# Performance work log

Hardware: AMD Instinct MI355X
Metric: run time of the kernel (lower is better)

## Reference

```python
import jax, jax.numpy as jnp
import numpy as np

B, S, H = 32768, 16, 16  # batch, seq_len, G_hiddensize (code requires H == S and H == latent_dim == 16)
LATENT = 16
DISC_DIMS = [(1, 32), (32, 16), (16, 8), (8, 16), (16, 32)]


def setup_inputs() -> dict:
    key = jax.random.key(0)
    ks = iter(jax.random.split(key, 64))
    def p(shape, scale=0.1):
        return (jax.random.normal(next(ks), shape, dtype=jnp.float32) * scale)
    inp = dict(
        values=jax.random.normal(next(ks), (B, S), dtype=jnp.float32),
        masks=jax.random.randint(next(ks), (B, S), 0, 2).astype(jnp.int32),
        g_fwd_Wih=p((4 * H, 1)), g_fwd_Whh=p((4 * H, H)), g_fwd_b=p((4 * H,)),
        g_bwd_Wih=p((4 * H, 1)), g_bwd_Whh=p((4 * H, H)), g_bwd_b=p((4 * H,)),
        imp_W=p((1, H)), imp_b=p((1,)),
        fc_W=p((LATENT, H)), fc_b=p((LATENT,)),
        dec_Wih=p((4 * H, LATENT)), dec_Whh=p((4 * H, H)), dec_b=p((4 * H,)),
        dec_out_W=p((1, H)), dec_out_b=p((1,)),
        disc_out_W=p((1, 32)), disc_out_b=p((1,)),
    )
    for k, (i, h) in enumerate(DISC_DIMS):
        inp[f"d_W_{k}"] = p((4 * h, i))
        inp[f"d_b_{k}"] = p((4 * h,))
    return inp


def lstm_cell(x, h, c, Wih, Whh, b):
    gates = x @ Wih.T + h @ Whh.T + b
    i, f, g, o = jnp.split(gates, 4, axis=-1)
    c = jax.nn.sigmoid(f) * c + jax.nn.sigmoid(i) * jnp.tanh(g)
    h = jax.nn.sigmoid(o) * jnp.tanh(c)
    return h, c


def _forward(values, masks, g_fwd_Wih, g_fwd_Whh, g_fwd_b, g_bwd_Wih, g_bwd_Whh, g_bwd_b,
             imp_W, imp_b, fc_W, fc_b, dec_Wih, dec_Whh, dec_b, dec_out_W, dec_out_b,
             disc_out_W, disc_out_b,
             d_W_0, d_b_0, d_W_1, d_b_1, d_W_2, d_b_2, d_W_3, d_b_3, d_W_4, d_b_4):
    dt = values.dtype
    Bsz = values.shape[0]
    x = values[:, :, None]                     # (B, S, 1)
    m = masks.astype(dt)[:, :, None]           # (B, S, 1)
    # NOTE: torch.flip along axis 2 (size 1) is a no-op, so the bwd cell sees the
    # same (un-reversed) sequence as the fwd cell -- faithfully reproduced here.
    zH = jnp.zeros((Bsz, H), dt)
    h_f, c_f = lstm_cell(jnp.full((Bsz, 1), 128.0, dt), zH, zH, g_fwd_Wih, g_fwd_Whh, g_fwd_b)
    h_b, c_b = lstm_cell(jnp.full((Bsz, 1), -128.0, dt), zH, zH, g_bwd_Wih, g_bwd_Whh, g_bwd_b)

    def gen_step(carry, xm):
        h_f, c_f, h_b, c_b = carry
        x_t, m_t = xm                          # (B,1) each
        cc_f = (1 - m_t) * x_t + m_t * (h_f @ imp_W.T + imp_b)
        cc_b = (1 - m_t) * x_t + m_t * (h_b @ imp_W.T + imp_b)
        h_f, c_f = lstm_cell(cc_f, h_f, c_f, g_fwd_Wih, g_fwd_Whh, g_fwd_b)
        h_b, c_b = lstm_cell(cc_b, h_b, c_b, g_bwd_Wih, g_bwd_Whh, g_bwd_b)
        return (h_f, c_f, h_b, c_b), None

    (h_f, c_f, h_b, c_b), _ = jax.lax.scan(
        gen_step, (h_f, c_f, h_b, c_b),
        (jnp.transpose(x, (1, 0, 2)), jnp.transpose(m, (1, 0, 2))))
    h = h_f + h_b                               # (B, H), H == S
    imputations = h.reshape(Bsz, S, 1)
    imputed = imputations * (1 - m) + x * m      # (B, S, 1)

    # Discriminator: torch calls each LSTMCell WITHOUT state every timestep, so
    # hidden/cell start at zero each call -> purely feedforward per (batch, t).
    # W_hh @ 0 == 0, so only W_ih and the combined bias matter. Vectorize over B*S.
    inp = imputed.reshape(Bsz * S, 1)
    for W, b in ((d_W_0, d_b_0), (d_W_1, d_b_1), (d_W_2, d_b_2), (d_W_3, d_b_3), (d_W_4, d_b_4)):
        gates = inp @ W.T + b
        i, f, g, o = jnp.split(gates, 4, axis=-1)
        cc = jax.nn.sigmoid(i) * jnp.tanh(g)
        inp = jax.nn.sigmoid(o) * jnp.tanh(cc)
    disc_output = (inp @ disc_out_W.T + disc_out_b).reshape(Bsz, S, 1)

    latent = h @ fc_W.T + fc_b                  # (B, 16)

    # Decoder: ignores latent values (only uses batch size); start token = 128s.
    hd = cd = jnp.zeros((Bsz, H), dt)
    hd, cd = lstm_cell(jnp.full((Bsz, LATENT), 128.0, dt), hd, cd, dec_Wih, dec_Whh, dec_b)

    def dec_step(carry, _):
        hd, cd = carry
        hd, cd = lstm_cell(cd, hd, cd, dec_Wih, dec_Whh, dec_b)
        return (hd, cd), hd @ dec_out_W.T + dec_out_b

    _, outs = jax.lax.scan(dec_step, (hd, cd), None, length=S)  # (S, B, 1)
    reconstructed = jnp.transpose(outs, (1, 0, 2))
    return imputed, disc_output, latent, reconstructed


def reference(values, masks, g_fwd_Wih, g_fwd_Whh, g_fwd_b, g_bwd_Wih, g_bwd_Whh, g_bwd_b,
              imp_W, imp_b, fc_W, fc_b, dec_Wih, dec_Whh, dec_b, dec_out_W, dec_out_b,
              disc_out_W, disc_out_b,
              d_W_0, d_b_0, d_W_1, d_b_1, d_W_2, d_b_2, d_W_3, d_b_3, d_W_4, d_b_4):
    return _forward(values, masks, g_fwd_Wih, g_fwd_Whh, g_fwd_b, g_bwd_Wih, g_bwd_Whh, g_bwd_b,
                    imp_W, imp_b, fc_W, fc_b, dec_Wih, dec_Whh, dec_b, dec_out_W, dec_out_b,
                    disc_out_W, disc_out_b,
                    d_W_0, d_b_0, d_W_1, d_b_1, d_W_2, d_b_2, d_W_3, d_b_3, d_W_4, d_b_4)
```

## Files before the change

kernel.cpp:

```cpp
#include <hip/hip_runtime.h>

#define BB 32768
#define BS (BB*16)

typedef __attribute__((ext_vector_type(8))) short bf8v;
typedef __attribute__((ext_vector_type(4))) float f4v;

#define RECO 64
#define TAB  128
#define NTAB 2049
#define HFO  8448
#define HBO  (HFO+BS)

#define PW0 0
#define PB0 96
#define PW1 192
#define PB1 1920
#define PW2 1968
#define PB2 2448
#define PW3 2472
#define PB3 3048
#define PW4 3096
#define PB4 5016
#define POW 5112
#define POB 5144
#define PN  5148

#define NSCAN 1024
#define NTABB 129
#define DECB  (NSCAN + NTABB)

__device__ __forceinline__ float sigm(float x){
    return __builtin_amdgcn_rcpf(1.f + __expf(-x));
}
__device__ __forceinline__ float tanh_f(float x){
    return 1.f - 2.f * __builtin_amdgcn_rcpf(1.f + __expf(2.f * x));
}
__device__ __forceinline__ float dunit(float gi, float gg, float go){
    return sigm(go) * tanh_f(sigm(gi) * tanh_f(gg));
}
__device__ __forceinline__ unsigned short f2bf(float f){
    union { float f; unsigned int i; } v; v.f = f;
    unsigned int x = v.i;
    unsigned int r = x + 0x7fffu + ((x >> 16) & 1u);
    return (unsigned short)(r >> 16);
}

struct P29 { const float* p[29]; };

__device__ __forceinline__ bf8v makeB(const float* Whh, const float* Wih,
                                      int row, int quad)
{
    bf8v B = {0,0,0,0,0,0,0,0};
    if (quad < 2) {
        const float4* p = (const float4*)(Whh + row*16 + quad*8);
        float4 a0 = p[0], a1 = p[1];
        B[0]=(short)f2bf(a0.x); B[1]=(short)f2bf(a0.y);
        B[2]=(short)f2bf(a0.z); B[3]=(short)f2bf(a0.w);
        B[4]=(short)f2bf(a1.x); B[5]=(short)f2bf(a1.y);
        B[6]=(short)f2bf(a1.z); B[7]=(short)f2bf(a1.w);
    } else if (quad == 2) {
        B[0] = (short)f2bf(Wih[row]);
    }
    return B;
}

__global__ __launch_bounds__(256)
void k_main(P29 a, const int* __restrict__ masks, float* __restrict__ ws)
{
    __shared__ __align__(16) float smem[PN];
    int tid = threadIdx.x;

    if (blockIdx.x < NSCAN) {
        int lane = tid & 63;
        int wv   = tid >> 6;
        int n    = lane & 15;
        int quad = lane >> 4;
        int dir  = (int)(blockIdx.x >= 512);
        int gid0 = blockIdx.x * 64 + wv * 16;
        int b0   = gid0 & 32767;
        float* wbase = smem + wv * 656;
        float* xs    = wbase;
        int*   msI   = (int*)(wbase + 256);
        unsigned short* hbp = (unsigned short*)(wbase + 512);
        float* ccf   = wbase + 640;
        const int4* hbI = (const int4*)hbp;
        {
            size_t gbase = (size_t)b0 * 16;
            int e = lane * 4;
            float4 xv = *(const float4*)(a.p[0] + gbase + e);
            int4   mv = *(const int4*)(masks + gbase + e);
            int sm = lane >> 2;
            int st = (lane & 3) * 4;
            xs[(st+0)*16 + sm] = xv.x;  msI[(st+0)*16 + sm] = mv.x;
            xs[(st+1)*16 + sm] = xv.y;  msI[(st+1)*16 + sm] = mv.y;
            xs[(st+2)*16 + sm] = xv.z;  msI[(st+2)*16 + sm] = mv.z;
            xs[(st+3)*16 + sm] = xv.w;  msI[(st+3)*16 + sm] = mv.w;
        }
        const float* __restrict__ Wih = a.p[2 + 3*dir];
        const float* __restrict__ Whh = a.p[3 + 3*dir];
        const float* __restrict__ bia = a.p[4 + 3*dir];
        bf8v Bi = makeB(Whh, Wih, n,      quad);
        bf8v Bf = makeB(Whh, Wih, 16+n,   quad);
        bf8v Bg = makeB(Whh, Wih, 32+n,   quad);
        bf8v Bo = makeB(Whh, Wih, 48+n,   quad);
        bf8v Bp = {0,0,0,0,0,0,0,0};
        if (quad < 2) {
            const float4* p = (const float4*)(a.p[8] + quad*8);
            float4 a0 = p[0], a1 = p[1];
            Bp[0]=(short)f2bf(a0.x); Bp[1]=(short)f2bf(a0.y);
            Bp[2]=(short)f2bf(a0.z); Bp[3]=(short)f2bf(a0.w);
            Bp[4]=(short)f2bf(a1.x); Bp[5]=(short)f2bf(a1.y);
            Bp[6]=(short)f2bf(a1.z); Bp[7]=(short)f2bf(a1.w);
        }
        float impb = a.p[9][0];
        float bi_ = bia[n], bf_ = bia[16+n], bg_ = bia[32+n], bo_ = bia[48+n];
        float sgn = dir ? -128.f : 128.f;
        float c0, h0;
        {
            float gi0 = sgn*Wih[n]    + bi_;
            float gg0 = sgn*Wih[32+n] + bg_;
            float go0 = sgn*Wih[48+n] + bo_;
            c0 = sigm(gi0) * tanh_f(gg0);
            h0 = sigm(go0) * tanh_f(c0);
        }
        float c[4] = {c0, c0, c0, c0};
        float h[4];
        {
            unsigned short hb0 = f2bf(h0);
            #pragma unroll
            for (int r = 0; r < 4; r++) hbp[(quad*4+r)*16 + n] = hb0;
        }
        const f4v cz = {0.f, 0.f, 0.f, 0.f};
        const bf8v Az = {0,0,0,0,0,0,0,0};
        for (int t = 0; t < 16; t++) {
            union { int4 i4; bf8v b; } au;
            au.i4 = hbI[(n << 1) | (quad & 1)];
            bf8v A = (quad < 2) ? au.b : Az;
            f4v dimp = __builtin_amdgcn_mfma_f32_16x16x32_bf16(A, Bp, cz, 0, 0, 0);
            float4 xt4 = *(const float4*)(xs + t*16 + quad*4);
            int4   mt4 = *(const int4*)(msI + t*16 + quad*4);
            float cc0 = mt4.x ? (dimp[0] + impb) : xt4.x;
            float cc1 = mt4.y ? (dimp[1] + impb) : xt4.y;
            float cc2 = mt4.z ? (dimp[2] + impb) : xt4.z;
            float cc3 = mt4.w ? (dimp[3] + impb) : xt4.w;
            if (n == 0) {
                ccf[quad*4+0] = cc0; ccf[quad*4+1] = cc1;
                ccf[quad*4+2] = cc2; ccf[quad*4+3] = cc3;
            }
            if (quad == 2) A[0] = (short)f2bf(ccf[n]);
            f4v di = __builtin_amdgcn_mfma_f32_16x16x32_bf16(A, Bi, cz, 0, 0, 0);
            f4v df = __builtin_amdgcn_mfma_f32_16x16x32_bf16(A, Bf, cz, 0, 0, 0);
            f4v dg = __builtin_amdgcn_mfma_f32_16x16x32_bf16(A, Bg, cz, 0, 0, 0);
            f4v dO = __builtin_amdgcn_mfma_f32_16x16x32_bf16(A, Bo, cz, 0, 0, 0);
            #pragma unroll
            for (int r = 0; r < 4; r++) {
                float gi = di[r] + bi_;
                float gf = df[r] + bf_;
                float gg = dg[r] + bg_;
                float go = dO[r] + bo_;
                float cn = sigm(gf)*c[r] + sigm(gi)*tanh_f(gg);
                c[r] = cn;
                float hh = sigm(go)*tanh_f(cn);
                h[r] = hh;
                hbp[(quad*4+r)*16 + n] = f2bf(hh);
            }
        }
        float* outp = ws + HFO + (size_t)dir*BS + (size_t)b0*16;
        #pragma unroll
        for (int r = 0; r < 4; r++) outp[(quad*4+r)*16 + n] = h[r];
        return;
    }

    if (blockIdx.x < DECB) {
        float* wl = smem;
#define STAGE(WS, BSi, h, K, padK, wdst, bdst) \
    { const float* Wp = a.p[WS]; const float* Bp2 = a.p[BSi]; \
      for (int i = tid; i < 3*(h)*(K); i += 256){ \
        int r = i/(K), k = i - r*(K); int g = r/(h), u0 = r - g*(h); \
        int sr = (g==0? u0 : (g==1? 2*(h)+u0 : 3*(h)+u0)); \
        wl[(wdst) + r*(padK) + k] = Wp[sr*(K) + k]; } \
      for (int i = tid; i < 3*(h); i += 256){ \
        int g = i/(h), u0 = i - g*(h); \
        int sr = (g==0? u0 : (g==1? 2*(h)+u0 : 3*(h)+u0)); \
        wl[(bdst) + i] = Bp2[sr]; } }
        STAGE(19, 20, 32,  1,  1, PW0, PB0)
        STAGE(21, 22, 16, 32, 36, PW1, PB1)
        STAGE(23, 24,  8, 16, 20, PW2, PB2)
        STAGE(25, 26, 16,  8, 12, PW3, PB3)
        STAGE(27, 28, 32, 16, 20, PW4, PB4)
#undef STAGE
        { const float* s = a.p[17]; for (int i = tid; i < 32; i += 256) wl[POW+i] = s[i]; }
        if (tid == 0) wl[POB] = a.p[18][0];
        __syncthreads();
        int u = tid & 15;
        int gbase = (tid & 63) & 48;
        int gid = (blockIdx.x - NSCAN) * 16 + (tid >> 4);
        const float4* w4 = (const float4*)wl;
        float xin = -8.f + (float)gid * (1.f/128.f);
        float lo = dunit(xin*wl[PW0+u]    + wl[PB0+u],
                         xin*wl[PW0+32+u] + wl[PB0+32+u],
                         xin*wl[PW0+64+u] + wl[PB0+64+u]);
        float hi = dunit(xin*wl[PW0+16+u] + wl[PB0+16+u],
                         xin*wl[PW0+48+u] + wl[PB0+48+u],
                         xin*wl[PW0+80+u] + wl[PB0+80+u]);
        float A0[32];
        #pragma unroll
        for (int k = 0; k < 16; k++) { A0[k] = __shfl(lo, gbase+k); A0[16+k] = __shfl(hi, gbase+k); }
        float gi = wl[PB1+u], gg = wl[PB1+16+u], go = wl[PB1+32+u];
        int bi_ = (PW1 + u*36)>>2, bg_ = (PW1 + (16+u)*36)>>2, bo_ = (PW1 + (32+u)*36)>>2;
        #pragma unroll
        for (int q = 0; q < 8; q++) {
            float4 wi = w4[bi_+q], wg = w4[bg_+q], wo = w4[bo_+q];
            float b0=A0[4*q], b1=A0[4*q+1], b2=A0[4*q+2], b3=A0[4*q+3];
            gi += b0*wi.x + b1*wi.y + b2*wi.z + b3*wi.w;
            gg += b0*wg.x + b1*wg.y + b2*wg.z + b3*wg.w;
            go += b0*wo.x + b1*wo.y + b2*wo.z + b3*wo.w;
        }
        float a1 = dunit(gi, gg, go);
        float A1[16];
        #pragma unroll
        for (int k = 0; k < 16; k++) A1[k] = __shfl(a1, gbase+k);
        int v = u & 7;
        gi = wl[PB2+v]; gg = wl[PB2+8+v]; go = wl[PB2+16+v];
        bi_ = (PW2 + v*20)>>2; bg_ = (PW2 + (8+v)*20)>>2; bo_ = (PW2 + (16+v)*20)>>2;
        #pragma unroll
        for (int q = 0; q < 4; q++) {
            float4 wi = w4[bi_+q], wg = w4[bg_+q], wo = w4[bo_+q];
            float b0=A1[4*q], b1=A1[4*q+1], b2=A1[4*q+2], b3=A1[4*q+3];
            gi += b0*wi.x + b1*wi.y + b2*wi.z + b3*wi.w;
            gg += b0*wg.x + b1*wg.y + b2*wg.z + b3*wg.w;
            go += b0*wo.x + b1*wo.y + b2*wo.z + b3*wo.w;
        }
        float a2 = dunit(gi, gg, go);
        float A2[8];
        #pragma unroll
        for (int k = 0; k < 8; k++) A2[k] = __shfl(a2, gbase+k);
        gi = wl[PB3+u]; gg = wl[PB3+16+u]; go = wl[PB3+32+u];
        bi_ = (PW3 + u*12)>>2; bg_ = (PW3 + (16+u)*12)>>2; bo_ = (PW3 + (32+u)*12)>>2;
        #pragma unroll
        for (int q = 0; q < 2; q++) {
            float4 wi = w4[bi_+q], wg = w4[bg_+q], wo = w4[bo_+q];
            float b0=A2[4*q], b1=A2[4*q+1], b2=A2[4*q+2], b3=A2[4*q+3];
            gi += b0*wi.x + b1*wi.y + b2*wi.z + b3*wi.w;
            gg += b0*wg.x + b1*wg.y + b2*wg.z + b3*wg.w;
            go += b0*wo.x + b1*wo.y + b2*wo.z + b3*wo.w;
        }
        float a3 = dunit(gi, gg, go);
        float A3[16];
        #pragma unroll
        for (int k = 0; k < 16; k++) A3[k] = __shfl(a3, gbase+k);
        float part;
        {
            float g0i = wl[PB4+u], g0g = wl[PB4+32+u], g0o = wl[PB4+64+u];
            float g1i = wl[PB4+16+u], g1g = wl[PB4+48+u], g1o = wl[PB4+80+u];
            int c0i = (PW4 + u*20)>>2,      c0g = (PW4 + (32+u)*20)>>2, c0o = (PW4 + (64+u)*20)>>2;
            int c1i = (PW4 + (16+u)*20)>>2, c1g = (PW4 + (48+u)*20)>>2, c1o = (PW4 + (80+u)*20)>>2;
            #pragma unroll
            for (int q = 0; q < 4; q++) {
                float b0=A3[4*q], b1=A3[4*q+1], b2=A3[4*q+2], b3=A3[4*q+3];
                float4 wi = w4[c0i+q], wg = w4[c0g+q], wo = w4[c0o+q];
                g0i += b0*wi.x + b1*wi.y + b2*wi.z + b3*wi.w;
                g0g += b0*wg.x + b1*wg.y + b2*wg.z + b3*wg.w;
                g0o += b0*wo.x + b1*wo.y + b2*wo.z + b3*wo.w;
                wi = w4[c1i+q]; wg = w4[c1g+q]; wo = w4[c1o+q];
                g1i += b0*wi.x + b1*wi.y + b2*wi.z + b3*wi.w;
                g1g += b0*wg.x + b1*wg.y + b2*wg.z + b3*wg.w;
                g1o += b0*wo.x + b1*wo.y + b2*wo.z + b3*wo.w;
            }
            part = dunit(g0i, g0g, g0o)*wl[POW+u] + dunit(g1i, g1g, g1o)*wl[POW+16+u];
        }
        part += __shfl_xor(part, 1);
        part += __shfl_xor(part, 2);
        part += __shfl_xor(part, 4);
        part += __shfl_xor(part, 8);
        if (u == 0 && gid < NTAB) ws[TAB + gid] = part + wl[POB];
        return;
    }

    {
        float* dh = smem;
        float* dc = smem + 16;
        const float* Wih = a.p[12];
        const float* Whh = a.p[13];
        const float* bb  = a.p[14];
        const float* oW  = a.p[15];
        const float* ob  = a.p[16];
        float wii[16], wff[16], wgg[16], woo[16];
        float vii[16], vff[16], vgg[16], voo[16];
        float bi_r=0, bf_r=0, bg_r=0, bo_r=0;
        if (tid < 16) {
            int uu = tid;
            #pragma unroll
            for (int k = 0; k < 16; k++) {
                wii[k]=Wih[uu*16+k];      vii[k]=Whh[uu*16+k];
                wff[k]=Wih[(16+uu)*16+k]; vff[k]=Whh[(16+uu)*16+k];
                wgg[k]=Wih[(32+uu)*16+k]; vgg[k]=Whh[(32+uu)*16+k];
                woo[k]=Wih[(48+uu)*16+k]; voo[k]=Whh[(48+uu)*16+k];
            }
            bi_r=bb[uu]; bf_r=bb[16+uu]; bg_r=bb[32+uu]; bo_r=bb[48+uu];
            float gi = bi_r, gg = bg_r, go = bo_r;
            #pragma unroll
            for (int k = 0; k < 16; k++) {
                gi += 128.f * wii[k];
                gg += 128.f * wgg[k];
                go += 128.f * woo[k];
            }
            float cd0 = sigm(gi) * tanh_f(gg);
            dc[tid] = cd0; dh[tid] = sigm(go) * tanh_f(cd0);
        }
        __syncthreads();
        for (int t = 0; t < 16; t++) {
            float rx[16], rh[16], cold = 0.f;
            if (tid < 16) {
                #pragma unroll
                for (int k = 0; k < 16; k++) { rx[k] = dc[k]; rh[k] = dh[k]; }
                cold = dc[tid];
            }
            __syncthreads();
            if (tid < 16) {
                float gi = bi_r, gf = bf_r, gg = bg_r, go = bo_r;
                #pragma unroll
                for (int k = 0; k < 16; k++) {
                    gi += rx[k]*wii[k] + rh[k]*vii[k];
                    gf += rx[k]*wff[k] + rh[k]*vff[k];
                    gg += rx[k]*wgg[k] + rh[k]*vgg[k];
                    go += rx[k]*woo[k] + rh[k]*voo[k];
                }
                float cn = sigm(gf)*cold + sigm(gi)*tanh_f(gg);
                dc[tid] = cn; dh[tid] = sigm(go)*tanh_f(cn);
            }
            __syncthreads();
            if (tid == 0) {
                float o = ob[0];
                #pragma unroll
                for (int k = 0; k < 16; k++) o += dh[k] * oW[k];
                ws[RECO + t] = o;
            }
            __syncthreads();
        }
    }
}

__global__ __launch_bounds__(256) void k_post(P29 a, const int* __restrict__ masks,
                                              const float* __restrict__ ws,
                                              float* __restrict__ out)
{
    __shared__ float tab[NTAB];
    __shared__ __align__(16) float fw[256];
    __shared__ __align__(16) float rec[16];
    __shared__ float fb[16];
    int tid = threadIdx.x;
    for (int i = tid; i < NTAB; i += 256) tab[i] = ws[TAB + i];
    fw[tid] = a.p[10][tid];
    if (tid < 16) { fb[tid] = a.p[11][tid]; rec[tid] = ws[RECO + tid]; }
    __syncthreads();
    int T = blockIdx.x * 256 + tid;
    int b = T >> 2;
    int q = T & 3;
    int tq = q * 4;
    const float4* hf4 = (const float4*)(ws + HFO + (size_t)b*16);
    const float4* hb4 = (const float4*)(ws + HBO + (size_t)b*16);
    float4 s0, s1, s2, s3;
    {
        float4 f0=hf4[0], f1=hf4[1], f2=hf4[2], f3=hf4[3];
        float4 g0=hb4[0], g1=hb4[1], g2=hb4[2], g3=hb4[3];
        s0 = make_float4(f0.x+g0.x, f0.y+g0.y, f0.z+g0.z, f0.w+g0.w);
        s1 = make_float4(f1.x+g1.x, f1.y+g1.y, f1.z+g1.z, f1.w+g1.w);
        s2 = make_float4(f2.x+g2.x, f2.y+g2.y, f2.z+g2.z, f2.w+g2.w);
        s3 = make_float4(f3.x+g3.x, f3.y+g3.y, f3.z+g3.z, f3.w+g3.w);
    }
    float4 hq = (q==0) ? s0 : (q==1) ? s1 : (q==2) ? s2 : s3;
    float4 xv = *(const float4*)(a.p[0] + (size_t)b*16 + tq);
    int4   mv = *(const int4*)(masks + (size_t)b*16 + tq);
    float impv[4];
    impv[0] = mv.x ? xv.x : hq.x;
    impv[1] = mv.y ? xv.y : hq.y;
    impv[2] = mv.z ? xv.z : hq.z;
    impv[3] = mv.w ? xv.w : hq.w;
    float latv[4];
    #pragma unroll
    for (int j = 0; j < 4; j++) {
        int t = tq + j;
        const float4* wr = (const float4*)(fw + t*16);
        float4 w0=wr[0], w1=wr[1], w2=wr[2], w3=wr[3];
        float l = fb[t];
        l += s0.x*w0.x + s0.y*w0.y + s0.z*w0.z + s0.w*w0.w;
        l += s1.x*w1.x + s1.y*w1.y + s1.z*w1.z + s1.w*w1.w;
        l += s2.x*w2.x + s2.y*w2.y + s2.z*w2.z + s2.w*w2.w;
        l += s3.x*w3.x + s3.y*w3.y + s3.z*w3.z + s3.w*w3.w;
        latv[j] = l;
    }
    float dv[4];
    #pragma unroll
    for (int j = 0; j < 4; j++) {
        float xx = fminf(fmaxf(impv[j], -8.f), 8.f);
        float f = (xx + 8.f) * 128.f;
        float fi = floorf(f);
        int i = (int)fi; i = i > NTAB-2 ? NTAB-2 : i;
        float w = f - fi;
        dv[j] = fmaf(w, tab[i+1] - tab[i], tab[i]);
    }
    float4 rv = ((const float4*)rec)[q];
    size_t eo = (size_t)b*16 + tq;
    *(float4*)(out + eo)        = make_float4(impv[0], impv[1], impv[2], impv[3]);
    *(float4*)(out + BS + eo)   = make_float4(dv[0], dv[1], dv[2], dv[3]);
    *(float4*)(out + 2*BS + eo) = make_float4(latv[0], latv[1], latv[2], latv[3]);
    *(float4*)(out + 3*BS + eo) = rv;
}

extern "C" void kernel_launch(void* const* d_in, const int* in_sizes, int n_in,
                              void* d_out, int out_size, void* d_ws, size_t ws_size,
                              hipStream_t stream)
{
    float* ws = (float*)d_ws;
    P29 a;
    for (int i = 0; i < 29; i++) a.p[i] = (const float*)d_in[i];
    const int* masks = (const int*)d_in[1];
    k_main<<<NSCAN + NTABB + 1, 256, 0, stream>>>(a, masks, ws);
    k_post<<<(BB*4)/256, 256, 0, stream>>>(a, masks, ws, (float*)d_out);
}
```

Baseline: 163.6 us.

## Store discriminator weights as bf16 in LDS and pad scan LDS rows

The discriminator table blocks now stage their weights in shared memory as bf16 and unpack them with shifts, which roughly halves the LDS footprint. The per-wave scan buffers are padded (row strides 20 and 24) to reduce bank conflicts on the transposed x/mask and hidden-state accesses. Together these shrink the block's static shared memory from about 20 KB to about 13.5 KB, so more blocks can be resident per CU. The cost is lower-precision discriminator weights in the table and extra unpack ALU work.

```diff
diff --git a/kernel.cpp b/kernel.cpp
--- a/kernel.cpp
+++ b/kernel.cpp
@@ -24,7 +24,10 @@
 #define PB4 5016
 #define POW 5112
 #define POB 5144
-#define PN  5148
+#define PNU 5148
+
+#define WVF 848
+#define SMF 3392
 
 #define NSCAN 1024
 #define NTABB 129
@@ -44,6 +47,15 @@
     unsigned int x = v.i;
     unsigned int r = x + 0x7fffu + ((x >> 16) & 1u);
     return (unsigned short)(r >> 16);
+}
+__device__ __forceinline__ float bfu(unsigned short s){
+    union { unsigned u; float f; } v; v.u = ((unsigned)s) << 16; return v.f;
+}
+__device__ __forceinline__ float bflo(unsigned p){
+    union { unsigned u; float f; } v; v.u = p << 16; return v.f;
+}
+__device__ __forceinline__ float bfhi(unsigned p){
+    union { unsigned u; float f; } v; v.u = p & 0xffff0000u; return v.f;
 }
 
 struct P29 { const float* p[29]; };
@@ -68,7 +80,7 @@
 __global__ __launch_bounds__(256)
 void k_main(P29 a, const int* __restrict__ masks, float* __restrict__ ws)
 {
-    __shared__ __align__(16) float smem[PN];
+    __shared__ __align__(16) float smem[SMF];
     int tid = threadIdx.x;
 
     if (blockIdx.x < NSCAN) {
@@ -79,11 +91,11 @@
         int dir  = (int)(blockIdx.x >= 512);
         int gid0 = blockIdx.x * 64 + wv * 16;
         int b0   = gid0 & 32767;
-        float* wbase = smem + wv * 656;
+        float* wbase = smem + wv * WVF;
         float* xs    = wbase;
-        int*   msI   = (int*)(wbase + 256);
-        unsigned short* hbp = (unsigned short*)(wbase + 512);
-        float* ccf   = wbase + 640;
+        int*   msI   = (int*)(wbase + 320);
+        unsigned short* hbp = (unsigned short*)(wbase + 640);
+        float* ccf   = wbase + 832;
         const int4* hbI = (const int4*)hbp;
         {
             size_t gbase = (size_t)b0 * 16;
@@ -92,10 +104,10 @@
             int4   mv = *(const int4*)(masks + gbase + e);
             int sm = lane >> 2;
             int st = (lane & 3) * 4;
-            xs[(st+0)*16 + sm] = xv.x;  msI[(st+0)*16 + sm] = mv.x;
-            xs[(st+1)*16 + sm] = xv.y;  msI[(st+1)*16 + sm] = mv.y;
-            xs[(st+2)*16 + sm] = xv.z;  msI[(st+2)*16 + sm] = mv.z;
-            xs[(st+3)*16 + sm] = xv.w;  msI[(st+3)*16 + sm] = mv.w;
+            xs[(st+0)*20 + sm] = xv.x;  msI[(st+0)*20 + sm] = mv.x;
+            xs[(st+1)*20 + sm] = xv.y;  msI[(st+1)*20 + sm] = mv.y;
+            xs[(st+2)*20 + sm] = xv.z;  msI[(st+2)*20 + sm] = mv.z;
+            xs[(st+3)*20 + sm] = xv.w;  msI[(st+3)*20 + sm] = mv.w;
         }
         const float* __restrict__ Wih = a.p[2 + 3*dir];
         const float* __restrict__ Whh = a.p[3 + 3*dir];
@@ -129,17 +141,17 @@
         {
             unsigned short hb0 = f2bf(h0);
             #pragma unroll
-            for (int r = 0; r < 4; r++) hbp[(quad*4+r)*16 + n] = hb0;
+            for (int r = 0; r < 4; r++) hbp[(quad*4+r)*24 + n] = hb0;
         }
         const f4v cz = {0.f, 0.f, 0.f, 0.f};
         const bf8v Az = {0,0,0,0,0,0,0,0};
         for (int t = 0; t < 16; t++) {
             union { int4 i4; bf8v b; } au;
-            au.i4 = hbI[(n << 1) | (quad & 1)];
+            au.i4 = hbI[n*3 + (quad & 1)];
             bf8v A = (quad < 2) ? au.b : Az;
             f4v dimp = __builtin_amdgcn_mfma_f32_16x16x32_bf16(A, Bp, cz, 0, 0, 0);
-            float4 xt4 = *(const float4*)(xs + t*16 + quad*4);
-            int4   mt4 = *(const int4*)(msI + t*16 + quad*4);
+            float4 xt4 = *(const float4*)(xs + t*20 + quad*4);
+            int4   mt4 = *(const int4*)(msI + t*20 + quad*4);
             float cc0 = mt4.x ? (dimp[0] + impb) : xt4.x;
             float cc1 = mt4.y ? (dimp[1] + impb) : xt4.y;
             float cc2 = mt4.z ? (dimp[2] + impb) : xt4.z;
@@ -163,7 +175,7 @@
                 c[r] = cn;
                 float hh = sigm(go)*tanh_f(cn);
                 h[r] = hh;
-                hbp[(quad*4+r)*16 + n] = f2bf(hh);
+                hbp[(quad*4+r)*24 + n] = f2bf(hh);
             }
         }
         float* outp = ws + HFO + (size_t)dir*BS + (size_t)b0*16;
@@ -173,78 +185,78 @@
     }
 
     if (blockIdx.x < DECB) {
-        float* wl = smem;
+        unsigned short* wl = (unsigned short*)smem;
 #define STAGE(WS, BSi, h, K, padK, wdst, bdst) \
     { const float* Wp = a.p[WS]; const float* Bp2 = a.p[BSi]; \
       for (int i = tid; i < 3*(h)*(K); i += 256){ \
         int r = i/(K), k = i - r*(K); int g = r/(h), u0 = r - g*(h); \
         int sr = (g==0? u0 : (g==1? 2*(h)+u0 : 3*(h)+u0)); \
-        wl[(wdst) + r*(padK) + k] = Wp[sr*(K) + k]; } \
+        wl[(wdst) + r*(padK) + k] = f2bf(Wp[sr*(K) + k]); } \
       for (int i = tid; i < 3*(h); i += 256){ \
         int g = i/(h), u0 = i - g*(h); \
         int sr = (g==0? u0 : (g==1? 2*(h)+u0 : 3*(h)+u0)); \
-        wl[(bdst) + i] = Bp2[sr]; } }
+        wl[(bdst) + i] = f2bf(Bp2[sr]); } }
         STAGE(19, 20, 32,  1,  1, PW0, PB0)
         STAGE(21, 22, 16, 32, 36, PW1, PB1)
         STAGE(23, 24,  8, 16, 20, PW2, PB2)
         STAGE(25, 26, 16,  8, 12, PW3, PB3)
         STAGE(27, 28, 32, 16, 20, PW4, PB4)
 #undef STAGE
-        { const float* s = a.p[17]; for (int i = tid; i < 32; i += 256) wl[POW+i] = s[i]; }
-        if (tid == 0) wl[POB] = a.p[18][0];
+        { const float* s = a.p[17]; for (int i = tid; i < 32; i += 256) wl[POW+i] = f2bf(s[i]); }
+        if (tid == 0) wl[POB] = f2bf(a.p[18][0]);
         __syncthreads();
         int u = tid & 15;
         int gbase = (tid & 63) & 48;
         int gid = (blockIdx.x - NSCAN) * 16 + (tid >> 4);
-        const float4* w4 = (const float4*)wl;
+        const uint2* w2 = (const uint2*)wl;
         float xin = -8.f + (float)gid * (1.f/128.f);
-        float lo = dunit(xin*wl[PW0+u]    + wl[PB0+u],
-                         xin*wl[PW0+32+u] + wl[PB0+32+u],
-                         xin*wl[PW0+64+u] + wl[PB0+64+u]);
-        float hi = dunit(xin*wl[PW0+16+u] + wl[PB0+16+u],
-                         xin*wl[PW0+48+u] + wl[PB0+48+u],
-                         xin*wl[PW0+80+u] + wl[PB0+80+u]);
+        float lo = dunit(xin*bfu(wl[PW0+u])    + bfu(wl[PB0+u]),
+                         xin*bfu(wl[PW0+32+u]) + bfu(wl[PB0+32+u]),
+                         xin*bfu(wl[PW0+64+u]) + bfu(wl[PB0+64+u]));
+        float hi = dunit(xin*bfu(wl[PW0+16+u]) + bfu(wl[PB0+16+u]),
+                         xin*bfu(wl[PW0+48+u]) + bfu(wl[PB0+48+u]),
+                         xin*bfu(wl[PW0+80+u]) + bfu(wl[PB0+80+u]));
         float A0[32];
         #pragma unroll
         for (int k = 0; k < 16; k++) { A0[k] = __shfl(lo, gbase+k); A0[16+k] = __shfl(hi, gbase+k); }
-        float gi = wl[PB1+u], gg = wl[PB1+16+u], go = wl[PB1+32+u];
+        float gi = bfu(wl[PB1+u]), gg = bfu(wl[PB1+16+u]), go = bfu(wl[PB1+32+u]);
         int bi_ = (PW1 + u*36)>>2, bg_ = (PW1 + (16+u)*36)>>2, bo_ = (PW1 + (32+u)*36)>>2;
         #pragma unroll
         for (int q = 0; q < 8; q++) {
-            float4 wi = w4[bi_+q], wg = w4[bg_+q], wo = w4[bo_+q];
+            uint2 wi = w2[bi_+q], wg = w2[bg_+q], wo = w2[bo_+q];
             float b0=A0[4*q], b1=A0[4*q+1], b2=A0[4*q+2], b3=A0[4*q+3];
-            gi += b0*wi.x + b1*wi.y + b2*wi.z + b3*wi.w;
-            gg += b0*wg.x + b1*wg.y + b2*wg.z + b3*wg.w;
-            go += b0*wo.x + b1*wo.y + b2*wo.z + b3*wo.w;
+            gi += b0*bflo(wi.x) + b1*bfhi(wi.x) + b2*bflo(wi.y) + b3*bfhi(wi.y);
+            gg += b0*bflo(wg.x) + b1*bfhi(wg.x) + b2*bflo(wg.y) + b3*bfhi(wg.y);
+            go += b0*bflo(wo.x) + b1*bfhi(wo.x) + b2*bflo(wo.y) + b3*bfhi(wo.y);
         }
         float a1 = dunit(gi, gg, go);
         float A1[16];
         #pragma unroll
         for (int k = 0; k < 16; k++) A1[k] = __shfl(a1, gbase+k);
         int v = u & 7;
-        gi = wl[PB2+v]; gg = wl[PB2+8+v]; go = wl[PB2+16+v];
+        gi = bfu(wl[PB2+v]); gg = bfu(wl[PB2+8+v]); go = bfu(wl[PB2+16+v]);
         bi_ = (PW2 + v*20)>>2; bg_ = (PW2 + (8+v)*20)>>2; bo_ = (PW2 + (16+v)*20)>>2;
         #pragma unroll
         for (int q = 0; q < 4; q++) {
-            float4 wi = w4[bi_+q], wg = w4[bg_+q], wo = w4[bo_+q];
+            uint2 wi = w2[bi_+q], wg = w2[bg_+q], wo = w2[bo_+q];
             float b0=A1[4*q], b1=A1[4*q+1], b2=A1[4*q+2], b3=A1[4*q+3];
-            gi += b0*wi.x + b1*wi.y + b2*wi.z + b3*wi.w;
-            gg += b0*wg.x + b1*wg.y + b2*wg.z + b3*wg.w;
-            go += b0*wo.x + b1*wo.y + b2*wo.z + b3*wo.w;
+            gi += b0*bflo(wi.x) + b1*bfhi(wi.x) + b2*bflo(wi.y) + b3*bfhi(wi.y);
+            gg += b0*bflo(wg.x) + b1*bfhi(wg.x) + b2*bflo(wg.y) + b3*bfhi(wg.y);
+            go += b0*bflo(wo.x) + b1*bfhi(wo.x) + b2*bflo(wo.y) + b3*bfhi(wo.y);
         }
         float a2 = dunit(gi, gg, go);
         float A2[8];
         #pragma unroll
         for (int k = 0; k < 8; k++) A2[k] = __shfl(a2, gbase+k);
-        gi = wl[PB3+u]; gg = wl[PB3+16+u]; go = wl[PB3+32+u];
+        gi = bfu(wl[PB3+u]); gg = bfu(wl[PB3+16+u]); go = bfu(wl[PB3+32+u]);
         bi_ = (PW3 + u*12)>>2; bg_ = (PW3 + (16+u)*12)>>2; bo_ = (PW3 + (32+u)*12)>>2;
         #pragma unroll
         for (int q = 0; q < 2; q++) {
-            float4 wi = w4[bi_+q], wg = w4[bg_+q], wo = w4[bo_+q];
+            uint2 wi = w2[bi_+q], wg = w2[bg_+q], wo = w2[bo_+q];
             float b0=A2[4*q], b1=A2[4*q+1], b2=A2[4*q+2], b3=A2[4*q+3];
-            gi += b0*wi.x + b1*wi.y + b2*wi.z + b3*wi.w;
-            gg += b0*wg.x + b1*wg.y + b2*wg.z + b3*wg.w;
-            go += b0*wo.x + b1*wo.y + b2*wo.z + b3*wo.w;
+            gi += b0*bflo(wi.x) + b1*bfhi(wi.x) + b2*bflo(wi.y) + b3*bfhi(wi.y);
+            gg += b0*bflo(wg.x) + b1*bfhi(wg.x) + b2*bflo(wg.y) + b3*bfhi(wg.y);
+            go += b0*bflo(wo.x) + b1*bfhi(wo.x) + b2*bflo(wo.y) + b3*bfhi(wo.y);
         }
         float a3 = dunit(gi, gg, go);
         float A3[16];
@@ -252,29 +264,29 @@
         for (int k = 0; k < 16; k++) A3[k] = __shfl(a3, gbase+k);
         float part;
         {
-            float g0i = wl[PB4+u], g0g = wl[PB4+32+u], g0o = wl[PB4+64+u];
-            float g1i = wl[PB4+16+u], g1g = wl[PB4+48+u], g1o = wl[PB4+80+u];
+            float g0i = bfu(wl[PB4+u]),    g0g = bfu(wl[PB4+32+u]), g0o = bfu(wl[PB4+64+u]);
+            float g1i = bfu(wl[PB4+16+u]), g1g = bfu(wl[PB4+48+u]), g1o = bfu(wl[PB4+80+u]);
             int c0i = (PW4 + u*20)>>2,      c0g = (PW4 + (32+u)*20)>>2, c0o = (PW4 + (64+u)*20)>>2;
             int c1i = (PW4 + (16+u)*20)>>2, c1g = (PW4 + (48+u)*20)>>2, c1o = (PW4 + (80+u)*20)>>2;
             #pragma unroll
             for (int q = 0; q < 4; q++) {
                 float b0=A3[4*q], b1=A3[4*q+1], b2=A3[4*q+2], b3=A3[4*q+3];
-                float4 wi = w4[c0i+q], wg = w4[c0g+q], wo = w4[c0o+q];
-                g0i += b0*wi.x + b1*wi.y + b2*wi.z + b3*wi.w;
-                g0g += b0*wg.x + b1*wg.y + b2*wg.z + b3*wg.w;
-                g0o += b0*wo.x + b1*wo.y + b2*wo.z + b3*wo.w;
-                wi = w4[c1i+q]; wg = w4[c1g+q]; wo = w4[c1o+q];
-                g1i += b0*wi.x + b1*wi.y + b2*wi.z + b3*wi.w;
-                g1g += b0*wg.x + b1*wg.y + b2*wg.z + b3*wg.w;
-                g1o += b0*wo.x + b1*wo.y + b2*wo.z + b3*wo.w;
-            }
-            part = dunit(g0i, g0g, g0o)*wl[POW+u] + dunit(g1i, g1g, g1o)*wl[POW+16+u];
+                uint2 wi = w2[c0i+q], wg = w2[c0g+q], wo = w2[c0o+q];
+                g0i += b0*bflo(wi.x) + b1*bfhi(wi.x) + b2*bflo(wi.y) + b3*bfhi(wi.y);
+                g0g += b0*bflo(wg.x) + b1*bfhi(wg.x) + b2*bflo(wg.y) + b3*bfhi(wg.y);
+                g0o += b0*bflo(wo.x) + b1*bfhi(wo.x) + b2*bflo(wo.y) + b3*bfhi(wo.y);
+                wi = w2[c1i+q]; wg = w2[c1g+q]; wo = w2[c1o+q];
+                g1i += b0*bflo(wi.x) + b1*bfhi(wi.x) + b2*bflo(wi.y) + b3*bfhi(wi.y);
+                g1g += b0*bflo(wg.x) + b1*bfhi(wg.x) + b2*bflo(wg.y) + b3*bfhi(wg.y);
+                g1o += b0*bflo(wo.x) + b1*bfhi(wo.x) + b2*bflo(wo.y) + b3*bfhi(wo.y);
+            }
+            part = dunit(g0i, g0g, g0o)*bfu(wl[POW+u]) + dunit(g1i, g1g, g1o)*bfu(wl[POW+16+u]);
         }
         part += __shfl_xor(part, 1);
         part += __shfl_xor(part, 2);
         part += __shfl_xor(part, 4);
         part += __shfl_xor(part, 8);
-        if (u == 0 && gid < NTAB) ws[TAB + gid] = part + wl[POB];
+        if (u == 0 && gid < NTAB) ws[TAB + gid] = part + bfu(wl[POB]);
         return;
     }
 
```

Measured after the change: 160.0 us. 2.2% less time.
